# Optimization experiments

Hardware: AMD Instinct MI355X
Metric: run time of the kernel (lower is better)

The kernel has to match this reference:

```python
import jax, jax.numpy as jnp
import numpy as np

S, D, H, G, DH = 2048, 4096, 32, 8, 128  # seq, d_in, heads, kv_groups, head_dim
GROUP = H // G


def rotate_half(x):
    x1, x2 = jnp.split(x, 2, axis=-1)
    return jnp.concatenate([-x2, x1], axis=-1)


def setup_inputs() -> dict:
    key = jax.random.key(0)
    ks = jax.random.split(key, 8)
    x = jax.random.normal(ks[0], (1, S, D), dtype=jnp.float32)
    # causal mask: True above the diagonal (positions to mask out)
    mask = jnp.triu(jnp.ones((S, S), dtype=bool), k=1)
    # standard RoPE tables
    inv_freq = 1.0 / (10000.0 ** (np.arange(0, DH, 2, dtype=np.float32) / DH))
    t = np.arange(S, dtype=np.float32)
    freqs = np.outer(t, inv_freq)                      # [S, DH/2]
    emb = np.concatenate([freqs, freqs], axis=-1)      # [S, DH]
    cos = jnp.asarray(np.cos(emb), dtype=jnp.float32)
    sin = jnp.asarray(np.sin(emb), dtype=jnp.float32)
    sc = 0.02
    Wq = jax.random.normal(ks[1], (D, H * DH), dtype=jnp.float32) * sc
    Wk = jax.random.normal(ks[2], (D, G * DH), dtype=jnp.float32) * sc
    Wv = jax.random.normal(ks[3], (D, G * DH), dtype=jnp.float32) * sc
    Wo = jax.random.normal(ks[4], (H * DH, D), dtype=jnp.float32) * sc
    return {"x": x, "mask": mask, "cos": cos, "sin": sin,
            "Wq": Wq, "Wk": Wk, "Wv": Wv, "Wo": Wo}


def reference(x, mask, cos, sin, Wq, Wk, Wv, Wo):
    xs = x[0]                                          # [S, D] (batch must be 1)
    q = (xs @ Wq).reshape(S, H, DH).transpose(1, 0, 2)   # [H, S, DH]
    k = (xs @ Wk).reshape(S, G, DH).transpose(1, 0, 2)   # [G, S, DH]
    v = (xs @ Wv).reshape(S, G, DH).transpose(1, 0, 2)   # [G, S, DH]
    # RoPE
    q = q * cos[None] + rotate_half(q) * sin[None]
    k = k * cos[None] + rotate_half(k) * sin[None]
    # GQA: repeat KV groups to match query heads
    k = jnp.repeat(k, GROUP, axis=0)                   # [H, S, DH]
    v = jnp.repeat(v, GROUP, axis=0)                   # [H, S, DH]
    scores = jnp.einsum('hsd,htd->hst', q, k)          # [H, S, S]
    scores = jnp.where(mask[None], -jnp.inf, scores)
    scores = scores / jnp.sqrt(jnp.float32(DH))
    w = jax.nn.softmax(scores, axis=-1)
    ctx = jnp.einsum('hst,htd->hsd', w, v)             # [H, S, DH]
    ctx = ctx.transpose(1, 0, 2).reshape(S, H * DH)
    out = ctx @ Wo                                     # [S, D]
    return out[None]                                   # [1, S, D]
```

## Files before the change

kernel.cpp:

```cpp
#include <hip/hip_runtime.h>
#include <hip/hip_bf16.h>
#include <cstdint>
#include <cstddef>

#define S 2048
#define D 4096
#define H 32
#define G 8
#define DH 128
#define HD (H*DH)
#define GD (G*DH)

typedef __bf16 bf16;
typedef __bf16 bf16x4 __attribute__((ext_vector_type(4)));
typedef __bf16 bf16x8 __attribute__((ext_vector_type(8)));
typedef float f32x4 __attribute__((ext_vector_type(4)));

__device__ __forceinline__ void gload16(const void* g, void* l) {
    __builtin_amdgcn_global_load_lds(
        (const __attribute__((address_space(1))) void*)g,
        (__attribute__((address_space(3))) void*)l, 16, 0, 0);
}

#define FENCE() asm volatile("" ::: "memory")
#define BARRIER() do { FENCE(); __builtin_amdgcn_s_barrier(); FENCE(); } while (0)
#define VMCNT(n)  asm volatile("s_waitcnt vmcnt(" #n ")" ::: "memory")
#define LGKM0()   do { asm volatile("s_waitcnt lgkmcnt(0)" ::: "memory"); \
                       __builtin_amdgcn_sched_barrier(0); } while (0)

__global__ __launch_bounds__(256) void cast_f32_bf16(const float* __restrict__ in,
                                                     bf16* __restrict__ out, int n4)
{
    int i = blockIdx.x * 256 + threadIdx.x;
    if (i < n4) {
        float4 v = reinterpret_cast<const float4*>(in)[i];
        bf16x4 o = { (bf16)v.x, (bf16)v.y, (bf16)v.z, (bf16)v.w };
        reinterpret_cast<bf16x4*>(out)[i] = o;
    }
}

template<bool IN_F32>
__global__ __launch_bounds__(256) void transpose_to_bf16(
    const void* __restrict__ in, bf16* __restrict__ out, int R, int C)
{
    const int r0 = blockIdx.y * 64 + (threadIdx.x & 7) * 8;
    const int c0 = blockIdx.x * 256 + (threadIdx.x >> 3) * 8;
    bf16 m[8][8];
    #pragma unroll
    for (int j = 0; j < 8; ++j) {
        if constexpr (IN_F32) {
            const float* p = (const float*)in + (size_t)(r0 + j) * C + c0;
            float4 a = *reinterpret_cast<const float4*>(p);
            float4 b = *reinterpret_cast<const float4*>(p + 4);
            m[j][0] = (bf16)a.x; m[j][1] = (bf16)a.y; m[j][2] = (bf16)a.z; m[j][3] = (bf16)a.w;
            m[j][4] = (bf16)b.x; m[j][5] = (bf16)b.y; m[j][6] = (bf16)b.z; m[j][7] = (bf16)b.w;
        } else {
            const bf16* p = (const bf16*)in + (size_t)(r0 + j) * C + c0;
            bf16x8 v = *reinterpret_cast<const bf16x8*>(p);
            #pragma unroll
            for (int i = 0; i < 8; ++i) m[j][i] = v[i];
        }
    }
    #pragma unroll
    for (int i = 0; i < 8; ++i) {
        bf16x8 ov;
        #pragma unroll
        for (int j = 0; j < 8; ++j) ov[j] = m[j][i];
        *reinterpret_cast<bf16x8*>(out + (size_t)(c0 + i) * R + r0) = ov;
    }
}

__global__ __launch_bounds__(256) void rope_inplace(bf16* __restrict__ Y,
                                                    const float* __restrict__ cosT,
                                                    const float* __restrict__ sinT,
                                                    int ncols, int total, float scale)
{
    int idx = blockIdx.x * 256 + threadIdx.x;
    if (idx >= total) return;
    int pairs = ncols >> 1;
    int s = idx / pairs;
    int p = idx - s * pairs;
    int head = p >> 6;
    int d = p & 63;
    size_t base = (size_t)s * ncols + head * DH;
    float c  = cosT[s * DH + d];
    float sn = sinT[s * DH + d];
    float a = (float)Y[base + d];
    float b = (float)Y[base + d + 64];
    Y[base + d]      = (bf16)((a * c - b * sn) * scale);
    Y[base + d + 64] = (bf16)((b * c + a * sn) * scale);
}

__global__ __launch_bounds__(512) void gemm8p(
    const bf16* __restrict__ A, const bf16* __restrict__ Bt,
    bf16* __restrict__ Qout, bf16* __restrict__ Kout, bf16* __restrict__ Vout,
    const float* __restrict__ WoIn, bf16* __restrict__ WotOut,
    int N, int K, int nbn, int ngemm)
{
    extern __shared__ char smem[];
    const int tid = threadIdx.x;

    if ((int)blockIdx.x >= ngemm) {
        const int tb = blockIdx.x - ngemm;
        const int r0 = tb * 64 + (tid & 7) * 8;
        #pragma unroll 1
        for (int pass = 0; pass < 8; ++pass) {
            const int c0 = pass * 512 + (tid >> 3) * 8;
            bf16 m[8][8];
            #pragma unroll
            for (int j = 0; j < 8; ++j) {
                const float* p = WoIn + (size_t)(r0 + j) * D + c0;
                float4 a = *reinterpret_cast<const float4*>(p);
                float4 b = *reinterpret_cast<const float4*>(p + 4);
                m[j][0] = (bf16)a.x; m[j][1] = (bf16)a.y; m[j][2] = (bf16)a.z; m[j][3] = (bf16)a.w;
                m[j][4] = (bf16)b.x; m[j][5] = (bf16)b.y; m[j][6] = (bf16)b.z; m[j][7] = (bf16)b.w;
            }
            #pragma unroll
            for (int i = 0; i < 8; ++i) {
                bf16x8 ov;
                #pragma unroll
                for (int j = 0; j < 8; ++j) ov[j] = m[j][i];
                *reinterpret_cast<bf16x8*>(WotOut + (size_t)(c0 + i) * HD + r0) = ov;
            }
        }
        return;
    }

    const int lane = tid & 63, wave = tid >> 6;
    const int wr = wave >> 2, wc = wave & 3;
    const int l15 = lane & 15, lhi = lane >> 4;
    const int r8 = lane >> 3, c8 = lane & 7;
    const int csw = ((c8 ^ r8) << 3);

    const int qq = ngemm >> 3;
    const int swz = (blockIdx.x & 7) * qq + (blockIdx.x >> 3);
    const int bm = (swz / nbn) * 256, bn = (swz % nbn) * 256;
    const int NT = K >> 6;

    auto stageA = [&](int buf, int h, int t) {
        #pragma unroll
        for (int L = 0; L < 2; ++L) {
            int row0 = L * 128 + h * 64 + wave * 8;
            gload16(A + (size_t)(bm + row0 + r8) * K + (t << 6) + csw,
                    smem + buf * 65536 + row0 * 128);
        }
    };
    auto stageB = [&](int buf, int h, int t) {
        #pragma unroll
        for (int L = 0; L < 2; ++L) {
            int row0 = h * 128 + L * 64 + wave * 8;
            gload16(Bt + (size_t)(bn + row0 + r8) * K + (t << 6) + csw,
                    smem + buf * 65536 + 32768 + row0 * 128);
        }
    };
    auto rdA = [&](const char* Ab, int mh, int ks, bf16x8* af) {
        #pragma unroll
        for (int m = 0; m < 4; ++m) {
            int row = wr * 128 + mh * 64 + m * 16 + l15;
            int ch = (ks * 4 + lhi) ^ (l15 & 7);
            af[m] = *reinterpret_cast<const bf16x8*>(Ab + row * 128 + ch * 16);
        }
    };
    auto rdB = [&](const char* Bb, int ks, bf16x8* bfv) {
        #pragma unroll
        for (int n = 0; n < 4; ++n) {
            int row = wc * 64 + n * 16 + l15;
            int ch = (ks * 4 + lhi) ^ (l15 & 7);
            bfv[n] = *reinterpret_cast<const bf16x8*>(Bb + row * 128 + ch * 16);
        }
    };

    f32x4 acc[8][4] = {};

    auto mm = [&](int mh, const bf16x8* af, const bf16x8* bfv) {
        LGKM0();
        __builtin_amdgcn_s_setprio(1);
        #pragma unroll
        for (int m = 0; m < 4; ++m)
            #pragma unroll
            for (int n = 0; n < 4; ++n)
                acc[mh * 4 + m][n] = __builtin_amdgcn_mfma_f32_16x16x32_bf16(
                    af[m], bfv[n], acc[mh * 4 + m][n], 0, 0, 0);
        __builtin_amdgcn_s_setprio(0);
    };

    stageA(0, 0, 0); stageA(0, 1, 0); stageB(0, 0, 0); stageB(0, 1, 0);
    stageA(1, 0, 1);
    VMCNT(2);
    BARRIER();

    const char* A0 = smem;
    const char* B0 = smem + 32768;
    const char* A1 = smem + 65536;
    const char* B1 = smem + 65536 + 32768;

    for (int j = 0; j < (NT >> 1); ++j) {
        const int tb = 2 * j + 1;
        const int t2 = (2 * j + 2 < NT) ? 2 * j + 2 : NT - 1;
        const int t3 = (2 * j + 3 < NT) ? 2 * j + 3 : NT - 1;
        bf16x8 af[4], bk0[4], bk1[4];

        rdB(B0, 0, bk0); rdA(A0, 0, 0, af);
        stageA(1, 1, tb);
        mm(0, af, bk0);
        BARRIER();

        rdB(B0, 1, bk1); rdA(A0, 0, 1, af);
        stageB(1, 0, tb);
        mm(0, af, bk1);
        BARRIER();

        rdA(A0, 1, 0, af);
        stageB(1, 1, tb);
        mm(1, af, bk0);
        BARRIER();

        rdA(A0, 1, 1, af);
        stageA(0, 0, t2);
        VMCNT(2);
        mm(1, af, bk1);
        BARRIER();

        rdB(B1, 0, bk0); rdA(A1, 0, 0, af);
        stageA(0, 1, t2);
        mm(0, af, bk0);
        BARRIER();

        rdB(B1, 1, bk1); rdA(A1, 0, 1, af);
        stageB(0, 0, t2);
        mm(0, af, bk1);
        BARRIER();

        rdA(A1, 1, 0, af);
        stageB(0, 1, t2);
        mm(1, af, bk0);
        BARRIER();

        rdA(A1, 1, 1, af);
        stageA(1, 0, t3);
        VMCNT(2);
        mm(1, af, bk1);
        BARRIER();
    }

    #pragma unroll
    for (int m = 0; m < 8; ++m) {
        int r0 = bm + wr * 128 + m * 16 + lhi * 4;
        #pragma unroll
        for (int n = 0; n < 4; ++n) {
            int c = bn + wc * 64 + n * 16 + l15;
            #pragma unroll
            for (int j = 0; j < 4; ++j) {
                bf16 v = (bf16)acc[m][n][j];
                if (bn < HD)
                    Qout[(size_t)(r0 + j) * HD + c] = v;
                else if (bn < HD + GD)
                    Kout[(size_t)(r0 + j) * GD + (c - HD)] = v;
                else
                    Vout[(size_t)(r0 + j) * GD + (c - HD - GD)] = v;
            }
        }
    }
}

__global__ __launch_bounds__(512, 2) void gemm3b(
    const bf16* __restrict__ A, const bf16* __restrict__ Bt,
    float* __restrict__ C, int N, int K, int nbn)
{
    extern __shared__ char smem[];
    const int tid = threadIdx.x, lane = tid & 63, wave = tid >> 6;
    const int wr = wave >> 1, wc = wave & 1;
    const int l15 = lane & 15, lhi = lane >> 4;
    const int r8 = lane >> 3, c8 = lane & 7;
    const int csw = ((c8 ^ r8) << 3);

    const int nwg = gridDim.x, qq = nwg >> 3;
    const int swz = (blockIdx.x & 7) * qq + (blockIdx.x >> 3);
    const int bm = (swz / nbn) * 256, bn = (swz % nbn) * 128;
    const int NT = K >> 6;

    auto stageA = [&](int buf, int L, int t) {
        int row0 = L * 64 + wave * 8;
        gload16(A + (size_t)(bm + row0 + r8) * K + (t << 6) + csw,
                smem + buf * 49152 + row0 * 128);
    };
    auto stageB = [&](int buf, int L, int t) {
        int row0 = L * 64 + wave * 8;
        gload16(Bt + (size_t)(bn + row0 + r8) * K + (t << 6) + csw,
                smem + buf * 49152 + 32768 + row0 * 128);
    };
    auto rdA = [&](const char* Ab, int ks, bf16x8* af) {
        #pragma unroll
        for (int m = 0; m < 4; ++m) {
            int row = wr * 64 + m * 16 + l15;
            int ch = (ks * 4 + lhi) ^ (l15 & 7);
            af[m] = *reinterpret_cast<const bf16x8*>(Ab + row * 128 + ch * 16);
        }
    };
    auto rdB = [&](const char* Bb, int ks, bf16x8* bfv) {
        #pragma unroll
        for (int n = 0; n < 4; ++n) {
            int row = wc * 64 + n * 16 + l15;
            int ch = (ks * 4 + lhi) ^ (l15 & 7);
            bfv[n] = *reinterpret_cast<const bf16x8*>(Bb + row * 128 + ch * 16);
        }
    };

    f32x4 acc[4][4] = {};

    #pragma unroll
    for (int L = 0; L < 4; ++L) stageA(0, L, 0);
    stageB(0, 0, 0); stageB(0, 1, 0);
    #pragma unroll
    for (int L = 0; L < 4; ++L) stageA(1, L, (1 < NT) ? 1 : 0);
    stageB(1, 0, (1 < NT) ? 1 : 0); stageB(1, 1, (1 < NT) ? 1 : 0);
    VMCNT(6);
    BARRIER();

    for (int t = 0; t < NT; ++t) {
        const char* Ab = smem + (t % 3) * 49152;
        const char* Bb = Ab + 32768;
        const int b2 = (t + 2) % 3;
        const int st = (t + 2 < NT) ? t + 2 : NT - 1;
        bf16x8 af[4], bk[4];

        rdB(Bb, 0, bk); rdA(Ab, 0, af);
        stageA(b2, 0, st); stageA(b2, 1, st);
        LGKM0();
        __builtin_amdgcn_s_setprio(1);
        #pragma unroll
        for (int m = 0; m < 4; ++m)
            #pragma unroll
            for (int n = 0; n < 4; ++n)
                acc[m][n] = __builtin_amdgcn_mfma_f32_16x16x32_bf16(af[m], bk[n], acc[m][n], 0, 0, 0);
        __builtin_amdgcn_s_setprio(0);

        rdB(Bb, 1, bk); rdA(Ab, 1, af);
        stageA(b2, 2, st); stageA(b2, 3, st);
        stageB(b2, 0, st); stageB(b2, 1, st);
        LGKM0();
        __builtin_amdgcn_s_setprio(1);
        #pragma unroll
        for (int m = 0; m < 4; ++m)
            #pragma unroll
            for (int n = 0; n < 4; ++n)
                acc[m][n] = __builtin_amdgcn_mfma_f32_16x16x32_bf16(af[m], bk[n], acc[m][n], 0, 0, 0);
        __builtin_amdgcn_s_setprio(0);

        VMCNT(6);
        BARRIER();
    }

    #pragma unroll
    for (int m = 0; m < 4; ++m) {
        int r0 = bm + wr * 64 + m * 16 + lhi * 4;
        #pragma unroll
        for (int n = 0; n < 4; ++n) {
            int c = bn + wc * 64 + n * 16 + l15;
            #pragma unroll
            for (int j = 0; j < 4; ++j)
                C[(size_t)(r0 + j) * N + c] = acc[m][n][j];
        }
    }
}

#define BM 128
#define BN 128
#define BK 32
#define LDSK 40

template<bool OUT_BF16>
__global__ __launch_bounds__(256) void gemm_aBf16(
    const bf16* __restrict__ A,
    const float* __restrict__ B0, const float* __restrict__ B1,
    void* __restrict__ C0, void* __restrict__ C1,
    int M, int N, int K)
{
    __shared__ alignas(16) bf16 Al[BM][LDSK];
    __shared__ alignas(16) bf16 Bt[BN][LDSK];

    const float* __restrict__ B = blockIdx.z ? B1 : B0;
    void* __restrict__ C = blockIdx.z ? C1 : C0;

    const int tid  = threadIdx.x;
    const int lane = tid & 63;
    const int wave = tid >> 6;
    const int wm = (wave >> 1) * 64;
    const int wn = (wave & 1) * 64;
    const int bm = blockIdx.y * BM;
    const int bn = blockIdx.x * BN;
    const int l15 = lane & 15;
    const int lhi = lane >> 4;

    f32x4 acc[4][4] = {};

    for (int k0 = 0; k0 < K; k0 += BK) {
        #pragma unroll
        for (int it = 0; it < 2; ++it) {
            int idx = it * 256 + tid;
            int row = idx >> 2;
            int ko  = idx & 3;
            bf16x8 v = *reinterpret_cast<const bf16x8*>(
                A + (size_t)(bm + row) * K + k0 + ko * 8);
            *reinterpret_cast<bf16x8*>(&Al[row][ko * 8]) = v;
        }
        {
            int n = tid & 127;
            int kbase = (tid >> 7) * 8;
            const float* bp = B + (size_t)k0 * N + bn + n;
            #pragma unroll
            for (int half = 0; half < 2; ++half) {
                bf16x8 v;
                #pragma unroll
                for (int j = 0; j < 8; ++j)
                    v[j] = (bf16)bp[(size_t)(half * 16 + kbase + j) * N];
                *reinterpret_cast<bf16x8*>(&Bt[n][half * 16 + kbase]) = v;
            }
        }
        __syncthreads();

        bf16x8 af[4], bfv[4];
        #pragma unroll
        for (int m = 0; m < 4; ++m)
            af[m] = *reinterpret_cast<const bf16x8*>(&Al[wm + m * 16 + l15][lhi * 8]);
        #pragma unroll
        for (int n = 0; n < 4; ++n)
            bfv[n] = *reinterpret_cast<const bf16x8*>(&Bt[wn + n * 16 + l15][lhi * 8]);
        #pragma unroll
        for (int m = 0; m < 4; ++m)
            #pragma unroll
            for (int n = 0; n < 4; ++n)
                acc[m][n] = __builtin_amdgcn_mfma_f32_16x16x32_bf16(
                    af[m], bfv[n], acc[m][n], 0, 0, 0);
        __syncthreads();
    }

    #pragma unroll
    for (int m = 0; m < 4; ++m) {
        int r0 = bm + wm + m * 16 + lhi * 4;
        #pragma unroll
        for (int n = 0; n < 4; ++n) {
            int c = bn + wn + n * 16 + l15;
            #pragma unroll
            for (int j = 0; j < 4; ++j) {
                if constexpr (OUT_BF16)
                    reinterpret_cast<bf16*>(C)[(size_t)(r0 + j) * N + c] = (bf16)acc[m][n][j];
                else
                    reinterpret_cast<float*>(C)[(size_t)(r0 + j) * N + c] = acc[m][n][j];
            }
        }
    }
}

#define QBLK 128
#define KVBLK 64
#define NQT (S/QBLK)

template<bool MASK>
__device__ __forceinline__ void attn_tile(
    int t0, int q0, int wave, int l15, int lhi,
    const bf16x8* qf, const char* Kl, const char* Vl, char* Plw,
    f32x4* o, float* m_i, float* l_i)
{
    f32x4 sc[4] = {};
    __builtin_amdgcn_s_setprio(1);
    #pragma unroll
    for (int n = 0; n < 4; ++n) {
        int row = n * 16 + l15;
        #pragma unroll
        for (int kk = 0; kk < 4; ++kk) {
            bf16x8 kf = *reinterpret_cast<const bf16x8*>(
                Kl + row * 256 + ((((kk * 4 + lhi)) ^ (l15 & 7)) << 4));
            sc[n] = __builtin_amdgcn_mfma_f32_16x16x32_bf16(qf[kk], kf, sc[n], 0, 0, 0);
        }
    }
    __builtin_amdgcn_s_setprio(0);

    float corr[4];
    #pragma unroll
    for (int j = 0; j < 4; ++j) {
        const int qr = q0 + wave * 16 + lhi * 4 + j;
        float vals[4];
        float mx = -1e30f;
        #pragma unroll
        for (int n = 0; n < 4; ++n) {
            float v = sc[n][j];
            if constexpr (MASK) {
                int t = t0 + n * 16 + l15;
                if (t > qr) v = -1e30f;
            }
            vals[n] = v;
            mx = fmaxf(mx, v);
        }
        #pragma unroll
        for (int ms = 1; ms < 16; ms <<= 1)
            mx = fmaxf(mx, __shfl_xor(mx, ms, 16));
        float mnew, cr;
        if (mx <= m_i[j] + 8.0f) { mnew = m_i[j]; cr = 1.0f; }
        else                     { mnew = mx; cr = __expf(m_i[j] - mnew); }
        float rsum = 0.f;
        #pragma unroll
        for (int n = 0; n < 4; ++n) {
            float p = __expf(vals[n] - mnew);
            rsum += p;
            int r = lhi * 4 + j;
            int off = ((r << 7) + ((n * 16 + l15) << 1)) ^ ((r & 7) << 4);
            *reinterpret_cast<bf16*>(Plw + off) = (bf16)p;
        }
        #pragma unroll
        for (int ms = 1; ms < 16; ms <<= 1)
            rsum += __shfl_xor(rsum, ms, 16);
        l_i[j] = l_i[j] * cr + rsum;
        m_i[j] = mnew;
        corr[j] = cr;
    }

    if ((corr[0] != 1.f) | (corr[1] != 1.f) | (corr[2] != 1.f) | (corr[3] != 1.f)) {
        #pragma unroll
        for (int n = 0; n < 8; ++n)
            #pragma unroll
            for (int j = 0; j < 4; ++j)
                o[n][j] *= corr[j];
    }

    __builtin_amdgcn_s_setprio(1);
    #pragma unroll
    for (int kk = 0; kk < 2; ++kk) {
        bf16x8 pf = *reinterpret_cast<const bf16x8*>(
            Plw + (l15 << 7) + ((((kk * 4 + lhi)) ^ (l15 & 7)) << 4));
        #pragma unroll
        for (int n = 0; n < 8; ++n) {
            int d = n * 16 + l15;
            bf16x8 vf = *reinterpret_cast<const bf16x8*>(
                Vl + (d << 7) + ((((kk * 4 + lhi)) ^ (d & 7)) << 4));
            o[n] = __builtin_amdgcn_mfma_f32_16x16x32_bf16(pf, vf, o[n], 0, 0, 0);
        }
    }
    __builtin_amdgcn_s_setprio(0);
}

__global__ __launch_bounds__(512) void flash_fwd4(
    const bf16* __restrict__ Q, const bf16* __restrict__ Kr,
    const bf16* __restrict__ VtG, bf16* __restrict__ ctx)
{
    extern __shared__ char fsm[];

    const int tid  = threadIdx.x;
    const int lane = tid & 63;
    const int wave = tid >> 6;
    const int l15 = lane & 15;
    const int lhi = lane >> 4;
    const int bid = blockIdx.x;
    const int qt = (NQT - 1) - (bid >> 5);
    const int h  = ((bid & 7) << 2) | ((bid >> 3) & 3);
    const int g  = h >> 2;
    const int q0 = qt * QBLK;
    char* Plw = fsm + 65536 + wave * 2048;

    bf16x8 qf[4];
    {
        const bf16* qp = Q + (size_t)(q0 + wave * 16 + l15) * HD + h * DH + lhi * 8;
        #pragma unroll
        for (int kk = 0; kk < 4; ++kk)
            qf[kk] = *reinterpret_cast<const bf16x8*>(qp + kk * 32);
    }

    f32x4 o[8] = {};
    float m_i[4] = { -1e30f, -1e30f, -1e30f, -1e30f };
    float l_i[4] = {};

    auto stage = [&](int t0, int buf) {
        char* Kl = fsm + buf * 32768;
        char* Vl = Kl + 16384;
        #pragma unroll
        for (int t = 0; t < 2; ++t) {
            int ch = t * 512 + tid;
            {
                int row = ch >> 4, ci = ch & 15;
                gload16(Kr + (size_t)(t0 + row) * GD + g * DH + ((ci ^ (row & 7)) << 3),
                        Kl + ch * 16);
            }
            {
                int d = ch >> 3, ci = ch & 7;
                gload16(VtG + (size_t)(g * DH + d) * S + t0 + ((ci ^ (d & 7)) << 3),
                        Vl + ch * 16);
            }
        }
    };

    const int nt = 2 * qt + 2;
    stage(0, 0);
    VMCNT(0);
    BARRIER();

    for (int it = 0; it < nt; ++it) {
        if (it + 1 < nt) stage((it + 1) * KVBLK, (it + 1) & 1);
        const char* Kl = fsm + (it & 1) * 32768;
        const char* Vl = Kl + 16384;
        if (it >= nt - 2)
            attn_tile<true>(it * KVBLK, q0, wave, l15, lhi, qf, Kl, Vl, Plw, o, m_i, l_i);
        else
            attn_tile<false>(it * KVBLK, q0, wave, l15, lhi, qf, Kl, Vl, Plw, o, m_i, l_i);
        VMCNT(0);
        BARRIER();
    }

    #pragma unroll
    for (int n = 0; n < 8; ++n) {
        int c = h * DH + n * 16 + l15;
        #pragma unroll
        for (int j = 0; j < 4; ++j) {
            int r = q0 + wave * 16 + lhi * 4 + j;
            ctx[(size_t)r * HD + c] = (bf16)(o[n][j] / l_i[j]);
        }
    }
}

extern "C" void kernel_launch(void* const* d_in, const int* in_sizes, int n_in,
                              void* d_out, int out_size, void* d_ws, size_t ws_size,
                              hipStream_t stream)
{
    const float* x    = (const float*)d_in[0];
    const float* cosT = (const float*)d_in[2];
    const float* sinT = (const float*)d_in[3];
    const float* Wq   = (const float*)d_in[4];
    const float* Wk   = (const float*)d_in[5];
    const float* Wv   = (const float*)d_in[6];
    const float* Wo   = (const float*)d_in[7];
    float* out = (float*)d_out;

    const size_t MB = (size_t)1 << 20;
    char* ws = (char*)d_ws;
    bf16* xb  = (bf16*)ws;
    bf16* ctx = (bf16*)(ws + 16 * MB);
    bf16* Qb  = (bf16*)d_out;
    bf16* Kb  = Qb + (size_t)S * HD;
    bf16* Vb  = Kb + (size_t)S * GD;
    bf16* VtG = Vb + (size_t)S * GD;

    const bool fast = ws_size >= 112 * MB;
    const float qscale = 0.08838834764831845f;

    hipFuncSetAttribute(reinterpret_cast<const void*>(&flash_fwd4),
                        hipFuncAttributeMaxDynamicSharedMemorySize, 81920);

    cast_f32_bf16<<<(S * D / 4 + 255) / 256, 256, 0, stream>>>(x, xb, S * D / 4);

    if (fast) {
        bf16* Wqkvt = (bf16*)(ws + 32 * MB);
        bf16* Wot   = (bf16*)(ws + 80 * MB);

        transpose_to_bf16<true><<<dim3(HD / 256, D / 64), 256, 0, stream>>>(Wq, Wqkvt, D, HD);
        transpose_to_bf16<true><<<dim3(GD / 256, D / 64), 256, 0, stream>>>(Wk, Wqkvt + (size_t)HD * D, D, GD);
        transpose_to_bf16<true><<<dim3(GD / 256, D / 64), 256, 0, stream>>>(Wv, Wqkvt + (size_t)(HD + GD) * D, D, GD);

        hipFuncSetAttribute(reinterpret_cast<const void*>(&gemm8p),
                            hipFuncAttributeMaxDynamicSharedMemorySize, 131072);
        hipFuncSetAttribute(reinterpret_cast<const void*>(&gemm3b),
                            hipFuncAttributeMaxDynamicSharedMemorySize, 147456);

        gemm8p<<<256, 512, 131072, stream>>>(
            xb, Wqkvt, Qb, Kb, Vb, Wo, Wot, HD + 2 * GD, D, 24, 192);

        rope_inplace<<<(S * HD / 2 + 255) / 256, 256, 0, stream>>>(Qb, cosT, sinT, HD, S * HD / 2, qscale);
        rope_inplace<<<(S * GD / 2 + 255) / 256, 256, 0, stream>>>(Kb, cosT, sinT, GD, S * GD / 2, 1.0f);

        transpose_to_bf16<false><<<dim3(GD / 256, S / 64), 256, 0, stream>>>(Vb, VtG, S, GD);

        flash_fwd4<<<NQT * H, 512, 81920, stream>>>(Qb, Kb, VtG, ctx);

        gemm3b<<<256, 512, 147456, stream>>>(ctx, Wot, out, D, HD, 32);
    } else {
        gemm_aBf16<true><<<dim3(HD / BN, S / BM, 1), 256, 0, stream>>>(
            xb, Wq, Wq, (void*)Qb, (void*)Qb, S, HD, D);
        gemm_aBf16<true><<<dim3(GD / BN, S / BM, 2), 256, 0, stream>>>(
            xb, Wk, Wv, (void*)Kb, (void*)Vb, S, GD, D);

        rope_inplace<<<(S * HD / 2 + 255) / 256, 256, 0, stream>>>(Qb, cosT, sinT, HD, S * HD / 2, qscale);
        rope_inplace<<<(S * GD / 2 + 255) / 256, 256, 0, stream>>>(Kb, cosT, sinT, GD, S * GD / 2, 1.0f);

        transpose_to_bf16<false><<<dim3(GD / 256, S / 64), 256, 0, stream>>>(Vb, VtG, S, GD);

        flash_fwd4<<<NQT * H, 512, 81920, stream>>>(Qb, Kb, VtG, ctx);

        gemm_aBf16<false><<<dim3(D / BN, S / BM, 1), 256, 0, stream>>>(
            ctx, Wo, Wo, (void*)out, (void*)out, S, D, HD);
    }

    (void)in_sizes; (void)n_in; (void)out_size; (void)ws_size;
}
```

Measured before the change: 350.7 us.

## Fuse prep and RoPE/V-transpose kernels, use exp2 softmax, reorder GEMM wait

Four changes. The x cast and the three weight transposes are merged into one launch, and the Q/K RoPE passes are merged with the V transpose into a second launch, which removes several small kernel launches and their tail gaps. The softmax scale now includes log2(e), so flash attention can use exp2f instead of __expf. In the QKV GEMM the last MFMA of each phase is issued before the vmcnt wait, so more compute overlaps the outstanding global loads. The fused kernels branch on block index and do scalar bf16 RoPE loads, which may be less efficient per element than the separate kernels.

```diff
diff --git a/kernel.cpp b/kernel.cpp
--- a/kernel.cpp
+++ b/kernel.cpp
@@ -27,6 +27,89 @@
 #define VMCNT(n)  asm volatile("s_waitcnt vmcnt(" #n ")" ::: "memory")
 #define LGKM0()   do { asm volatile("s_waitcnt lgkmcnt(0)" ::: "memory"); \
                        __builtin_amdgcn_sched_barrier(0); } while (0)
+
+__global__ __launch_bounds__(256) void prep_fused(
+    const float* __restrict__ x, bf16* __restrict__ xb,
+    const float* __restrict__ Wq, const float* __restrict__ Wk,
+    const float* __restrict__ Wv, bf16* __restrict__ Wqkvt)
+{
+    const int b = blockIdx.x, tid = threadIdx.x;
+    if (b < 512) {
+        int i = b * 4096 + tid;
+        #pragma unroll
+        for (int it = 0; it < 16; ++it, i += 256) {
+            float4 v = reinterpret_cast<const float4*>(x)[i];
+            bf16x4 o = { (bf16)v.x, (bf16)v.y, (bf16)v.z, (bf16)v.w };
+            reinterpret_cast<bf16x4*>(xb)[i] = o;
+        }
+        return;
+    }
+    const float* in; bf16* out; int Cc, bx, by;
+    if (b < 1536)      { int tb = b - 512;  in = Wq; out = Wqkvt;                       Cc = HD; bx = tb & 15; by = tb >> 4; }
+    else if (b < 1792) { int tb = b - 1536; in = Wk; out = Wqkvt + (size_t)HD * D;      Cc = GD; bx = tb & 3;  by = tb >> 2; }
+    else               { int tb = b - 1792; in = Wv; out = Wqkvt + (size_t)(HD+GD) * D; Cc = GD; bx = tb & 3;  by = tb >> 2; }
+    const int r0 = by * 64 + (tid & 7) * 8;
+    const int c0 = bx * 256 + (tid >> 3) * 8;
+    bf16 m[8][8];
+    #pragma unroll
+    for (int j = 0; j < 8; ++j) {
+        const float* p = in + (size_t)(r0 + j) * Cc + c0;
+        float4 a = *reinterpret_cast<const float4*>(p);
+        float4 bq = *reinterpret_cast<const float4*>(p + 4);
+        m[j][0] = (bf16)a.x;  m[j][1] = (bf16)a.y;  m[j][2] = (bf16)a.z;  m[j][3] = (bf16)a.w;
+        m[j][4] = (bf16)bq.x; m[j][5] = (bf16)bq.y; m[j][6] = (bf16)bq.z; m[j][7] = (bf16)bq.w;
+    }
+    #pragma unroll
+    for (int i = 0; i < 8; ++i) {
+        bf16x8 ov;
+        #pragma unroll
+        for (int j = 0; j < 8; ++j) ov[j] = m[j][i];
+        *reinterpret_cast<bf16x8*>(out + (size_t)(c0 + i) * D + r0) = ov;
+    }
+}
+
+__global__ __launch_bounds__(256) void rope_vt_fused(
+    bf16* __restrict__ Qb, bf16* __restrict__ Kb,
+    const bf16* __restrict__ Vb, bf16* __restrict__ VtG,
+    const float* __restrict__ cosT, const float* __restrict__ sinT, float qs)
+{
+    const int b = blockIdx.x, tid = threadIdx.x;
+    if (b < 20480) {
+        bf16* Y; int ncols, idx; float scale;
+        if (b < 16384) { Y = Qb; ncols = HD; idx = b * 256 + tid;           scale = qs; }
+        else           { Y = Kb; ncols = GD; idx = (b - 16384) * 256 + tid; scale = 1.0f; }
+        int pairs = ncols >> 1;
+        int s = idx / pairs;
+        int p = idx - s * pairs;
+        int head = p >> 6;
+        int d = p & 63;
+        size_t base = (size_t)s * ncols + head * DH;
+        float c  = cosT[s * DH + d];
+        float sn = sinT[s * DH + d];
+        float a = (float)Y[base + d];
+        float bb = (float)Y[base + d + 64];
+        Y[base + d]      = (bf16)((a * c - bb * sn) * scale);
+        Y[base + d + 64] = (bf16)((bb * c + a * sn) * scale);
+        return;
+    }
+    const int tb = b - 20480;
+    const int r0 = (tb >> 2) * 64 + (tid & 7) * 8;
+    const int c0 = (tb & 3) * 256 + (tid >> 3) * 8;
+    bf16 m[8][8];
+    #pragma unroll
+    for (int j = 0; j < 8; ++j) {
+        bf16x8 v = *reinterpret_cast<const bf16x8*>(Vb + (size_t)(r0 + j) * GD + c0);
+        #pragma unroll
+        for (int i = 0; i < 8; ++i) m[j][i] = v[i];
+    }
+    #pragma unroll
+    for (int i = 0; i < 8; ++i) {
+        bf16x8 ov;
+        #pragma unroll
+        for (int j = 0; j < 8; ++j) ov[j] = m[j][i];
+        *reinterpret_cast<bf16x8*>(VtG + (size_t)(c0 + i) * S + r0) = ov;
+    }
+}
 
 __global__ __launch_bounds__(256) void cast_f32_bf16(const float* __restrict__ in,
                                                      bf16* __restrict__ out, int n4)
@@ -217,8 +300,8 @@
 
         rdA(A0, 1, 1, af);
         stageA(0, 0, t2);
+        mm(1, af, bk1);
         VMCNT(2);
-        mm(1, af, bk1);
         BARRIER();
 
         rdB(B1, 0, bk0); rdA(A1, 0, 0, af);
@@ -238,8 +321,8 @@
 
         rdA(A1, 1, 1, af);
         stageA(1, 0, t3);
+        mm(1, af, bk1);
         VMCNT(2);
-        mm(1, af, bk1);
         BARRIER();
     }
 
@@ -497,11 +580,11 @@
             mx = fmaxf(mx, __shfl_xor(mx, ms, 16));
         float mnew, cr;
         if (mx <= m_i[j] + 8.0f) { mnew = m_i[j]; cr = 1.0f; }
-        else                     { mnew = mx; cr = __expf(m_i[j] - mnew); }
+        else                     { mnew = mx; cr = exp2f(m_i[j] - mnew); }
         float rsum = 0.f;
         #pragma unroll
         for (int n = 0; n < 4; ++n) {
-            float p = __expf(vals[n] - mnew);
+            float p = exp2f(vals[n] - mnew);
             rsum += p;
             int r = lhi * 4 + j;
             int off = ((r << 7) + ((n * 16 + l15) << 1)) ^ ((r & 7) << 4);
@@ -539,7 +622,7 @@
     __builtin_amdgcn_s_setprio(0);
 }
 
-__global__ __launch_bounds__(512) void flash_fwd4(
+__global__ __launch_bounds__(512) void flash_fwd5(
     const bf16* __restrict__ Q, const bf16* __restrict__ Kr,
     const bf16* __restrict__ VtG, bf16* __restrict__ ctx)
 {
@@ -639,38 +722,33 @@
     bf16* VtG = Vb + (size_t)S * GD;
 
     const bool fast = ws_size >= 112 * MB;
-    const float qscale = 0.08838834764831845f;
-
-    hipFuncSetAttribute(reinterpret_cast<const void*>(&flash_fwd4),
+    const float qscale = 0.08838834764831845f * 1.4426950408889634f;
+
+    hipFuncSetAttribute(reinterpret_cast<const void*>(&flash_fwd5),
                         hipFuncAttributeMaxDynamicSharedMemorySize, 81920);
-
-    cast_f32_bf16<<<(S * D / 4 + 255) / 256, 256, 0, stream>>>(x, xb, S * D / 4);
 
     if (fast) {
         bf16* Wqkvt = (bf16*)(ws + 32 * MB);
         bf16* Wot   = (bf16*)(ws + 80 * MB);
-
-        transpose_to_bf16<true><<<dim3(HD / 256, D / 64), 256, 0, stream>>>(Wq, Wqkvt, D, HD);
-        transpose_to_bf16<true><<<dim3(GD / 256, D / 64), 256, 0, stream>>>(Wk, Wqkvt + (size_t)HD * D, D, GD);
-        transpose_to_bf16<true><<<dim3(GD / 256, D / 64), 256, 0, stream>>>(Wv, Wqkvt + (size_t)(HD + GD) * D, D, GD);
 
         hipFuncSetAttribute(reinterpret_cast<const void*>(&gemm8p),
                             hipFuncAttributeMaxDynamicSharedMemorySize, 131072);
         hipFuncSetAttribute(reinterpret_cast<const void*>(&gemm3b),
                             hipFuncAttributeMaxDynamicSharedMemorySize, 147456);
 
+        prep_fused<<<2048, 256, 0, stream>>>(x, xb, Wq, Wk, Wv, Wqkvt);
+
         gemm8p<<<256, 512, 131072, stream>>>(
             xb, Wqkvt, Qb, Kb, Vb, Wo, Wot, HD + 2 * GD, D, 24, 192);
 
-        rope_inplace<<<(S * HD / 2 + 255) / 256, 256, 0, stream>>>(Qb, cosT, sinT, HD, S * HD / 2, qscale);
-        rope_inplace<<<(S * GD / 2 + 255) / 256, 256, 0, stream>>>(Kb, cosT, sinT, GD, S * GD / 2, 1.0f);
-
-        transpose_to_bf16<false><<<dim3(GD / 256, S / 64), 256, 0, stream>>>(Vb, VtG, S, GD);
-
-        flash_fwd4<<<NQT * H, 512, 81920, stream>>>(Qb, Kb, VtG, ctx);
+        rope_vt_fused<<<20608, 256, 0, stream>>>(Qb, Kb, Vb, VtG, cosT, sinT, qscale);
+
+        flash_fwd5<<<NQT * H, 512, 81920, stream>>>(Qb, Kb, VtG, ctx);
 
         gemm3b<<<256, 512, 147456, stream>>>(ctx, Wot, out, D, HD, 32);
     } else {
+        cast_f32_bf16<<<(S * D / 4 + 255) / 256, 256, 0, stream>>>(x, xb, S * D / 4);
+
         gemm_aBf16<true><<<dim3(HD / BN, S / BM, 1), 256, 0, stream>>>(
             xb, Wq, Wq, (void*)Qb, (void*)Qb, S, HD, D);
         gemm_aBf16<true><<<dim3(GD / BN, S / BM, 2), 256, 0, stream>>>(
@@ -681,7 +759,7 @@
 
         transpose_to_bf16<false><<<dim3(GD / 256, S / 64), 256, 0, stream>>>(Vb, VtG, S, GD);
 
-        flash_fwd4<<<NQT * H, 512, 81920, stream>>>(Qb, Kb, VtG, ctx);
+        flash_fwd5<<<NQT * H, 512, 81920, stream>>>(Qb, Kb, VtG, ctx);
 
         gemm_aBf16<false><<<dim3(D / BN, S / BM, 1), 256, 0, stream>>>(
             ctx, Wo, Wo, (void*)out, (void*)out, S, D, HD);
```

New measurement: 345.2 us. About the same (-1.6%).
